# Performance work log

Measured on AMD Instinct MI355X. Metric: run time of the kernel, lower is better.

## Reference

```python
import jax, jax.numpy as jnp
import numpy as np

TOPK = 10
NUM_CLASSES = 80
ALPHA = 0.5
BETA = 6.0
EPS = 1e-9
IOU_EPS = 1e-7


def _make_anchors(img=640, strides=(8, 16, 32)):
    pts = []
    for s in strides:
        n = img // s
        ax = (np.arange(n, dtype=np.float32) + 0.5) * s
        gy, gx = np.meshgrid(ax, ax, indexing='ij')
        pts.append(np.stack([gx.ravel(), gy.ravel()], axis=-1))
    return jnp.asarray(np.concatenate(pts, axis=0), dtype=jnp.float32)  # [8400, 2]


def setup_inputs() -> dict:
    key = jax.random.key(0)
    ks = jax.random.split(key, 8)
    bs, ng, nc = 32, 64, NUM_CLASSES
    anc_points = _make_anchors()
    na = anc_points.shape[0]  # 8400
    pd_scores = jax.random.uniform(ks[0], (bs, na, nc), dtype=jnp.float32)
    pwh = jax.random.uniform(ks[1], (bs, na, 2), minval=10.0, maxval=100.0)
    pxy = anc_points[None] + jax.random.normal(ks[2], (bs, na, 2)) * 8.0
    pd_bboxes = jnp.concatenate([pxy - pwh / 2, pxy + pwh / 2], axis=-1)
    gxy = jax.random.uniform(ks[3], (bs, ng, 2), minval=50.0, maxval=590.0)
    gwh = jax.random.uniform(ks[4], (bs, ng, 2), minval=20.0, maxval=200.0)
    gt_bboxes = jnp.clip(jnp.concatenate([gxy - gwh / 2, gxy + gwh / 2], axis=-1), 0.0, 640.0)
    gt_labels = jax.random.randint(ks[5], (bs, ng, 1), 0, nc)
    num_gt = jax.random.randint(ks[6], (bs,), 1, ng + 1)
    mask_gt = (jnp.arange(ng)[None, :] < num_gt[:, None])[..., None]  # bool [bs, ng, 1]
    return {"pd_scores": pd_scores, "pd_bboxes": pd_bboxes, "anc_points": anc_points,
            "gt_labels": gt_labels, "gt_bboxes": gt_bboxes, "mask_gt": mask_gt}


def _iou_xyxy(b1, b2):
    # b1: [bs, na, 1, 4], b2: [bs, 1, ng, 4] -> [bs, na, ng]
    inter_w = jnp.maximum(jnp.minimum(b1[..., 2], b2[..., 2]) - jnp.maximum(b1[..., 0], b2[..., 0]), 0.0)
    inter_h = jnp.maximum(jnp.minimum(b1[..., 3], b2[..., 3]) - jnp.maximum(b1[..., 1], b2[..., 1]), 0.0)
    inter = inter_w * inter_h
    a1 = (b1[..., 2] - b1[..., 0]) * (b1[..., 3] - b1[..., 1])
    a2 = (b2[..., 2] - b2[..., 0]) * (b2[..., 3] - b2[..., 1])
    return inter / (a1 + a2 - inter + IOU_EPS)


def _assign(pd_scores, pd_bboxes, anc_points, gt_labels, gt_bboxes, mask_gt):
    bs, na, nc = pd_scores.shape
    ng = gt_bboxes.shape[1]
    dt = pd_scores.dtype

    # --- candidates whose center lies strictly inside the GT box ---
    lt = gt_bboxes[:, None, :, :2]          # [bs,1,ng,2]
    rb = gt_bboxes[:, None, :, 2:]
    xy = anc_points[None, :, None, :]       # [1,na,1,2]
    deltas = jnp.concatenate([xy - lt, rb - xy], axis=-1)  # [bs,na,ng,4]
    mask_in_gts = deltas.min(axis=-1) > EPS                 # [bs,na,ng]
    valid = mask_gt[..., 0].astype(bool)                    # [bs,ng]
    mask = mask_in_gts & valid[:, None, :]

    # --- alignment metric = score[label]^alpha * iou^beta, zeroed outside mask ---
    labels = gt_labels[..., 0].astype(jnp.int32)            # [bs,ng]
    idx = jnp.broadcast_to(labels[:, None, :], (bs, na, ng))
    gathered = jnp.take_along_axis(pd_scores, idx, axis=2)  # [bs,na,ng]
    bbox_scores = jnp.where(mask, gathered, 0.0)
    overlaps = jnp.where(mask, _iou_xyxy(pd_bboxes[:, :, None, :], gt_bboxes[:, None, :, :]), 0.0)
    safe_scores = jnp.where(mask, gathered, 1.0)  # avoids 0**0.5 grad issues; masked out below
    align_metric = jnp.where(mask, safe_scores ** ALPHA * overlaps ** BETA, 0.0)

    # --- top-k anchors per GT (over anchor dim) ---
    k = min(TOPK, na)
    _, topk_idx = jax.lax.top_k(jnp.swapaxes(align_metric, 1, 2), k)  # [bs,ng,k]
    bidx = jnp.arange(bs)[:, None, None]
    gidx = jnp.arange(ng)[None, :, None]
    in_topk = jnp.zeros((bs, ng, na), dtype=bool).at[bidx, gidx, topk_idx].set(True)
    in_topk = jnp.swapaxes(in_topk, 1, 2) & valid[:, None, :]  # [bs,na,ng]
    mask_pos = (in_topk & mask).astype(dt)

    # --- resolve anchors assigned to multiple GTs by highest IoU ---
    multi = mask_pos.sum(-1, keepdims=True) > 1
    is_max = jax.nn.one_hot(jnp.argmax(overlaps, axis=-1), ng, dtype=dt)
    mask_pos = jnp.where(multi, is_max, mask_pos)
    fg_mask = mask_pos.sum(-1) > 0                  # [bs,na] bool
    target_gt_idx = jnp.argmax(mask_pos, axis=-1)   # [bs,na]

    # --- gather targets ---
    flat_idx = target_gt_idx + jnp.arange(bs)[:, None] * ng
    target_labels = jnp.maximum(gt_labels[..., 0].reshape(-1)[flat_idx], 0)  # [bs,na]
    target_bboxes = gt_bboxes.reshape(-1, 4)[flat_idx]                       # [bs,na,4]
    one_hot = jax.nn.one_hot(target_labels, nc, dtype=dt) * fg_mask[..., None].astype(dt)

    fgf = fg_mask[..., None].astype(dt)
    norm_align = jnp.maximum((align_metric * fgf).max(-1, keepdims=True), EPS)
    norm_overlap = jnp.maximum((overlaps * fgf).max(-1, keepdims=True), EPS)
    t_scores = ((align_metric / norm_align) * (overlaps / norm_overlap) * fgf).max(-1)  # [bs,na]
    target_scores = one_hot * t_scores[..., None]
    return target_labels, target_bboxes, target_scores, fg_mask, target_gt_idx


def reference(pd_scores, pd_bboxes, anc_points, gt_labels, gt_bboxes, mask_gt):
    return _assign(pd_scores, pd_bboxes, anc_points, gt_labels, gt_bboxes, mask_gt)
```

## Files before the change

### kernel.cpp

```cpp
#include <hip/hip_runtime.h>
#include <math.h>

#define NC 80
#define TOPKK 10
#define EPSF 1e-9f
#define IOU_EPSF 1e-7f
#define NA 8400
#define NGMAX 64

__device__ __forceinline__ float iou_xyxy(float px0, float py0, float px1, float py1,
                                          float parea,
                                          float gx0, float gy0, float gx1, float gy1,
                                          float garea) {
    float iw = fmaxf(fminf(px1, gx1) - fmaxf(px0, gx0), 0.0f);
    float ih = fmaxf(fminf(py1, gy1) - fmaxf(py0, gy0), 0.0f);
    float inter = iw * ih;
    return inter / (parea + garea - inter + IOU_EPSF);
}

__device__ __forceinline__ float align_metric(float s, float ov) {
    float ov2 = ov * ov;
    return sqrtf(s) * (ov2 * ov2 * ov2);
}

__global__ __launch_bounds__(256) void topk_kernel(
    const float* __restrict__ pd_scores, const float* __restrict__ pd_bboxes,
    const float* __restrict__ anc, const int* __restrict__ gt_labels,
    const float* __restrict__ gt_bboxes, const int* __restrict__ mask_gt,
    unsigned long long* __restrict__ bits, int ng, int swz)
{
    __shared__ unsigned long long wkey[2][4];

    int b, g;
    if (swz) {
        int x = blockIdx.x & 7;
        int j = blockIdx.x >> 3;
        b = x * swz + j / ng;
        g = j - (j / ng) * ng;
    } else {
        b = blockIdx.x / ng;
        g = blockIdx.x - b * ng;
    }
    if (mask_gt[b * ng + g] == 0) return;

    int lab = gt_labels[b * ng + g];
    const float4 gb = ((const float4*)gt_bboxes)[b * ng + g];
    float gx0 = gb.x, gy0 = gb.y, gx1 = gb.z, gy1 = gb.w;
    float garea = (gx1 - gx0) * (gy1 - gy0);

    const float* __restrict__ srow = pd_scores + ((long)b * NA) * NC + lab;
    const float4* __restrict__ pbb = (const float4*)(pd_bboxes + (long)b * NA * 4);

    float lv[TOPKK];
    int   li[TOPKK];
#pragma unroll
    for (int j = 0; j < TOPKK; ++j) { lv[j] = -1.0f; li[j] = -1; }

    for (int a = threadIdx.x; a < NA; a += 256) {
        float ax = anc[a * 2 + 0];
        float ay = anc[a * 2 + 1];
        float d0 = ax - gx0, d1 = ay - gy0, d2 = gx1 - ax, d3 = gy1 - ay;
        float dmin = fminf(fminf(d0, d1), fminf(d2, d3));
        float v = 0.0f;
        if (dmin > EPSF) {
            float4 pb = pbb[a];
            float parea = (pb.z - pb.x) * (pb.w - pb.y);
            float ov = iou_xyxy(pb.x, pb.y, pb.z, pb.w, parea, gx0, gy0, gx1, gy1, garea);
            float s = srow[(long)a * NC];
            v = align_metric(s, ov);
        }
        if (v > lv[TOPKK - 1]) {
            float nv[TOPKK]; int ni[TOPKK];
#pragma unroll
            for (int j = 0; j < TOPKK; ++j) {
                bool keep = (lv[j] >= v);
                bool atp  = (j == 0) ? !keep : (!keep && (lv[j - 1] >= v));
                nv[j] = keep ? lv[j] : (atp ? v : lv[j - 1]);
                ni[j] = keep ? li[j] : (atp ? a : li[j - 1]);
            }
#pragma unroll
            for (int j = 0; j < TOPKK; ++j) { lv[j] = nv[j]; li[j] = ni[j]; }
        }
    }

    int lane = threadIdx.x & 63;
    int wid  = threadIdx.x >> 6;
    long bbase = (long)b * NA;

    for (int it = 0; it < TOPKK; ++it) {
        unsigned vb = __float_as_uint(lv[0]);
        unsigned long long myk = (lv[0] < 0.0f) ? 0ull
            : (((unsigned long long)vb << 32) | (unsigned)(~(unsigned)li[0]));

        unsigned long long k = myk;
#pragma unroll
        for (int off = 32; off > 0; off >>= 1) {
            unsigned long long o = __shfl_xor(k, off, 64);
            k = (o > k) ? o : k;
        }
        if (lane == 0) wkey[it & 1][wid] = k;
        __syncthreads();
        unsigned long long gk = wkey[it & 1][0];
        gk = (wkey[it & 1][1] > gk) ? wkey[it & 1][1] : gk;
        gk = (wkey[it & 1][2] > gk) ? wkey[it & 1][2] : gk;
        gk = (wkey[it & 1][3] > gk) ? wkey[it & 1][3] : gk;

        if (gk != 0ull && myk == gk) {
            atomicOr(&bits[bbase + li[0]], 1ull << g);
#pragma unroll
            for (int j = 0; j < TOPKK - 1; ++j) { lv[j] = lv[j + 1]; li[j] = li[j + 1]; }
            lv[TOPKK - 1] = -1.0f; li[TOPKK - 1] = -1;
        }
    }
}

__global__ __launch_bounds__(256) void assign_scores_kernel(
    const float* __restrict__ pd_scores, const float* __restrict__ pd_bboxes,
    const float* __restrict__ anc, const int* __restrict__ gt_labels,
    const float* __restrict__ gt_bboxes, const int* __restrict__ mask_gt,
    const unsigned long long* __restrict__ bits,
    float* __restrict__ out_labels, float* __restrict__ out_bboxes,
    float* __restrict__ out_scores, float* __restrict__ out_fg,
    float* __restrict__ out_tgt, int ng, int blocksPerB)
{
    __shared__ float4 sgt[NGMAX];
    __shared__ float  sarea[NGMAX];
    __shared__ int    slab[NGMAX];
    __shared__ int    svalid[NGMAX];
    __shared__ int    plab[256];
    __shared__ float  pt[256];

    int b  = blockIdx.x / blocksPerB;
    int a0 = (blockIdx.x - b * blocksPerB) * 256;
    int a  = a0 + threadIdx.x;

    for (int g = threadIdx.x; g < ng; g += 256) {
        float4 gb = ((const float4*)gt_bboxes)[b * ng + g];
        sgt[g] = gb;
        sarea[g] = (gb.z - gb.x) * (gb.w - gb.y);
        slab[g] = gt_labels[b * ng + g];
        svalid[g] = mask_gt[b * ng + g];
    }
    __syncthreads();

    bool alive = (a < NA);
    int labi = 0; float t = 0.0f;

    if (alive) {
        float ax = anc[a * 2 + 0];
        float ay = anc[a * 2 + 1];
        float4 pb = ((const float4*)pd_bboxes)[(long)b * NA + a];
        float parea = (pb.z - pb.x) * (pb.w - pb.y);
        unsigned long long w = bits[(long)b * NA + a];
        const float* __restrict__ srow = pd_scores + ((long)b * NA + a) * NC;

        int cnt = 0, pos_g = 0;
        float best_ov = 0.0f; int best_g = 0;
        float m_align = 0.0f, m_ov = 0.0f, t_raw = 0.0f;

        for (int g = 0; g < ng; ++g) {
            if (svalid[g] == 0) break;
            float4 gb = sgt[g];
            float d0 = ax - gb.x, d1 = ay - gb.y, d2 = gb.z - ax, d3 = gb.w - ay;
            float dmin = fminf(fminf(d0, d1), fminf(d2, d3));
            bool mask = (dmin > EPSF);
            float ov = 0.0f, al = 0.0f;
            if (mask) {
                ov = iou_xyxy(pb.x, pb.y, pb.z, pb.w, parea, gb.x, gb.y, gb.z, gb.w, sarea[g]);
                float s = srow[slab[g]];
                al = align_metric(s, ov);
            }
            bool pos = mask && ((w >> g) & 1ull);
            if (pos) { if (cnt == 0) pos_g = g; cnt++; }
            if (ov > best_ov) { best_ov = ov; best_g = g; }
            m_align = fmaxf(m_align, al);
            m_ov    = fmaxf(m_ov, ov);
            t_raw   = fmaxf(t_raw, al * ov);
        }

        int fg  = (cnt > 0) ? 1 : 0;
        int tgt = (cnt > 1) ? best_g : ((cnt == 1) ? pos_g : 0);

        labi = slab[tgt]; if (labi < 0) labi = 0;
        long ba = (long)b * NA + a;
        out_labels[ba] = (float)labi;
        ((float4*)out_bboxes)[ba] = sgt[tgt];
        out_fg[ba]  = (float)fg;
        out_tgt[ba] = (float)tgt;

        if (fg) {
            float na_ = fmaxf(m_align, EPSF);
            float no_ = fmaxf(m_ov, EPSF);
            t = (t_raw / na_) / no_;
        }
    }

    plab[threadIdx.x] = labi;
    pt[threadIdx.x]   = t;
    __syncthreads();

    int cnt_rows = NA - a0; if (cnt_rows > 256) cnt_rows = 256;
    int tot4 = cnt_rows * (NC / 4);
    float4* __restrict__ oslab = (float4*)(out_scores + ((long)b * NA + a0) * NC);
    for (int i = threadIdx.x; i < tot4; i += 256) {
        int al = i / (NC / 4);
        int cg = (i - al * (NC / 4)) * 4;
        int lab = plab[al];
        float tv = pt[al];
        float4 o;
        o.x = (cg     == lab) ? tv : 0.0f;
        o.y = (cg + 1 == lab) ? tv : 0.0f;
        o.z = (cg + 2 == lab) ? tv : 0.0f;
        o.w = (cg + 3 == lab) ? tv : 0.0f;
        oslab[i] = o;
    }
}

extern "C" void kernel_launch(void* const* d_in, const int* in_sizes, int n_in,
                              void* d_out, int out_size, void* d_ws, size_t ws_size,
                              hipStream_t stream) {
    const float* pd_scores = (const float*)d_in[0];
    const float* pd_bboxes = (const float*)d_in[1];
    const float* anc       = (const float*)d_in[2];
    const int*   gt_labels = (const int*)d_in[3];
    const float* gt_bboxes = (const float*)d_in[4];
    const int*   mask_gt   = (const int*)d_in[5];

    int na = in_sizes[2] / 2;
    int bs = in_sizes[0] / (na * NC);
    int ng = in_sizes[3] / bs;

    long nBA = (long)bs * na;
    float* out        = (float*)d_out;
    float* out_labels = out;
    float* out_bboxes = out + nBA;
    float* out_scores = out + nBA * 5;
    float* out_fg     = out + nBA * 85;
    float* out_tgt    = out + nBA * 86;

    unsigned long long* bits = (unsigned long long*)d_ws;

    hipMemsetAsync(d_ws, 0, nBA * sizeof(unsigned long long), stream);

    int swz = (bs % 8 == 0) ? (bs / 8) : 0;
    topk_kernel<<<bs * ng, 256, 0, stream>>>(
        pd_scores, pd_bboxes, anc, gt_labels, gt_bboxes, mask_gt, bits, ng, swz);

    int bpb = (na + 255) / 256;
    assign_scores_kernel<<<bs * bpb, 256, 0, stream>>>(
        pd_scores, pd_bboxes, anc, gt_labels, gt_bboxes, mask_gt, bits,
        out_labels, out_bboxes, out_scores, out_fg, out_tgt, ng, bpb);
}
```

Before: 205.3 us.

## Split top-k into anchor-chunk local selection plus per-GT merge phase

Replaces the per-(batch,GT) top-k kernel with two phases. The first phase stages a 128-anchor chunk of scores and boxes in shared memory and computes local top-10 lists for all 64 GTs at once. The second phase merges the per-chunk candidates with wave shuffles and sets the assignment bits. This removes 64 redundant strided passes over pd_scores per batch, at the cost of a large candidate buffer in workspace and an extra launch. The assign kernel also skips per-GT work for anchors with no bits set and uses nontemporal stores for the score tensor.

```diff
diff --git a/kernel.cpp b/kernel.cpp
--- a/kernel.cpp
+++ b/kernel.cpp
@@ -7,6 +7,10 @@
 #define IOU_EPSF 1e-7f
 #define NA 8400
 #define NGMAX 64
+#define CH 128
+#define NCH ((NA + CH - 1) / CH)
+
+typedef float f4nt __attribute__((ext_vector_type(4)));
 
 __device__ __forceinline__ float iou_xyxy(float px0, float py0, float px1, float py1,
                                           float parea,
@@ -22,6 +26,175 @@
     float ov2 = ov * ov;
     return sqrtf(s) * (ov2 * ov2 * ov2);
 }
+
+
+__global__ __launch_bounds__(256) void topk_phase1(
+    const float* __restrict__ pd_scores, const float* __restrict__ pd_bboxes,
+    const float* __restrict__ anc, const int* __restrict__ gt_labels,
+    const float* __restrict__ gt_bboxes, const int* __restrict__ mask_gt,
+    unsigned long long* __restrict__ cand, int ng)
+{
+    __shared__ union {
+        float sc[CH * NC];
+        unsigned long long mk[NGMAX * 4 * TOPKK];
+    } U;
+    __shared__ float4 sbb[CH];
+    __shared__ float2 sanc[CH];
+    __shared__ float4 sgt[NGMAX];
+    __shared__ int    slab[NGMAX];
+    __shared__ int    svalid[NGMAX];
+
+    int b  = blockIdx.x / NCH;
+    int c  = blockIdx.x - b * NCH;
+    int a0 = c * CH;
+    int rows = NA - a0; if (rows > CH) rows = CH;
+
+    for (int g = threadIdx.x; g < NGMAX; g += 256) {
+        if (g < ng) {
+            sgt[g]    = ((const float4*)gt_bboxes)[b * ng + g];
+            slab[g]   = gt_labels[b * ng + g];
+            svalid[g] = mask_gt[b * ng + g];
+        } else {
+            sgt[g] = make_float4(0, 0, 0, 0); slab[g] = 0; svalid[g] = 0;
+        }
+    }
+    for (int i = threadIdx.x; i < rows; i += 256) {
+        sbb[i]  = ((const float4*)pd_bboxes)[(long)b * NA + a0 + i];
+        sanc[i] = ((const float2*)anc)[a0 + i];
+    }
+    {
+        const float4* src = (const float4*)(pd_scores + ((long)b * NA + a0) * NC);
+        float4* dst = (float4*)U.sc;
+        int n4 = rows * (NC / 4);
+        for (int i = threadIdx.x; i < n4; i += 256) dst[i] = src[i];
+    }
+    __syncthreads();
+
+    int g   = threadIdx.x & 63;
+    int sub = threadIdx.x >> 6;
+
+    float lv[TOPKK]; int li[TOPKK];
+#pragma unroll
+    for (int j = 0; j < TOPKK; ++j) { lv[j] = -1.0f; li[j] = -1; }
+
+    if (svalid[g] != 0) {
+        float4 gb = sgt[g];
+        float garea = (gb.z - gb.x) * (gb.w - gb.y);
+        int lab = slab[g];
+        for (int al = sub; al < rows; al += 4) {
+            float2 ap = sanc[al];
+            float d0 = ap.x - gb.x, d1 = ap.y - gb.y, d2 = gb.z - ap.x, d3 = gb.w - ap.y;
+            float dmin = fminf(fminf(d0, d1), fminf(d2, d3));
+            float v = 0.0f;
+            if (dmin > EPSF) {
+                float4 pb = sbb[al];
+                float parea = (pb.z - pb.x) * (pb.w - pb.y);
+                float ov = iou_xyxy(pb.x, pb.y, pb.z, pb.w, parea,
+                                    gb.x, gb.y, gb.z, gb.w, garea);
+                float s = U.sc[al * NC + lab];
+                v = align_metric(s, ov);
+            }
+            if (v > lv[TOPKK - 1]) {
+                int a = a0 + al;
+                float nv[TOPKK]; int ni[TOPKK];
+#pragma unroll
+                for (int j = 0; j < TOPKK; ++j) {
+                    bool keep = (lv[j] >= v);
+                    bool atp  = (j == 0) ? !keep : (!keep && (lv[j - 1] >= v));
+                    nv[j] = keep ? lv[j] : (atp ? v : lv[j - 1]);
+                    ni[j] = keep ? li[j] : (atp ? a : li[j - 1]);
+                }
+#pragma unroll
+                for (int j = 0; j < TOPKK; ++j) { lv[j] = nv[j]; li[j] = ni[j]; }
+            }
+        }
+    }
+
+    __syncthreads();
+#pragma unroll
+    for (int j = 0; j < TOPKK; ++j) {
+        unsigned long long k = (lv[j] < 0.0f) ? 0ull
+            : (((unsigned long long)__float_as_uint(lv[j]) << 32)
+               | (unsigned)(~(unsigned)li[j]));
+        U.mk[(g * 4 + sub) * TOPKK + j] = k;
+    }
+    __syncthreads();
+
+    if (threadIdx.x < 64) {
+        int gg = threadIdx.x;
+        const unsigned long long* L = &U.mk[gg * 4 * TOPKK];
+        unsigned long long* outp = &cand[(((long)b * NCH + c) * 64 + gg) * TOPKK];
+        int p0 = 0, p1 = 0, p2 = 0, p3 = 0;
+#pragma unroll
+        for (int j = 0; j < TOPKK; ++j) {
+            unsigned long long k0 = L[0 * TOPKK + p0], k1 = L[1 * TOPKK + p1];
+            unsigned long long k2 = L[2 * TOPKK + p2], k3 = L[3 * TOPKK + p3];
+            unsigned long long bk = k0; int bi = 0;
+            if (k1 > bk) { bk = k1; bi = 1; }
+            if (k2 > bk) { bk = k2; bi = 2; }
+            if (k3 > bk) { bk = k3; bi = 3; }
+            outp[j] = bk;
+            if (bk != 0ull) {
+                if (bi == 0) p0++; else if (bi == 1) p1++;
+                else if (bi == 2) p2++; else p3++;
+            }
+        }
+    }
+}
+
+__global__ __launch_bounds__(64) void topk_phase2(
+    const unsigned long long* __restrict__ cand, const int* __restrict__ mask_gt,
+    unsigned long long* __restrict__ bits, int ng)
+{
+    int b = blockIdx.x / ng;
+    int g = blockIdx.x - b * ng;
+    if (mask_gt[b * ng + g] == 0) return;
+    int lane = threadIdx.x;
+
+    unsigned long long A[TOPKK], B[TOPKK], M[TOPKK];
+    {
+        const unsigned long long* p = &cand[(((long)b * NCH + lane) * 64 + g) * TOPKK];
+#pragma unroll
+        for (int j = 0; j < TOPKK; ++j) A[j] = p[j];
+    }
+    int c2 = lane + 64;
+    if (c2 < NCH) {
+        const unsigned long long* p = &cand[(((long)b * NCH + c2) * 64 + g) * TOPKK];
+#pragma unroll
+        for (int j = 0; j < TOPKK; ++j) B[j] = p[j];
+    } else {
+#pragma unroll
+        for (int j = 0; j < TOPKK; ++j) B[j] = 0ull;
+    }
+    {
+        int pa = 0, pb = 0;
+#pragma unroll
+        for (int j = 0; j < TOPKK; ++j) {
+            unsigned long long ka = A[pa], kb = B[pb];
+            if (ka >= kb) { M[j] = ka; if (ka != 0ull) pa++; }
+            else          { M[j] = kb; pb++; }
+        }
+    }
+
+    int pos = 0;
+    long bbase = (long)b * NA;
+    for (int it = 0; it < TOPKK; ++it) {
+        unsigned long long myk = (pos < TOPKK) ? M[pos] : 0ull;
+        unsigned long long k = myk;
+#pragma unroll
+        for (int off = 32; off > 0; off >>= 1) {
+            unsigned long long o = __shfl_xor(k, off, 64);
+            k = (o > k) ? o : k;
+        }
+        if (k == 0ull) break;
+        if (myk == k) {
+            unsigned idx = ~(unsigned)k;
+            atomicOr(&bits[bbase + idx], 1ull << g);
+            pos++;
+        }
+    }
+}
+
 
 __global__ __launch_bounds__(256) void topk_kernel(
     const float* __restrict__ pd_scores, const float* __restrict__ pd_bboxes,
@@ -51,8 +224,7 @@
     const float* __restrict__ srow = pd_scores + ((long)b * NA) * NC + lab;
     const float4* __restrict__ pbb = (const float4*)(pd_bboxes + (long)b * NA * 4);
 
-    float lv[TOPKK];
-    int   li[TOPKK];
+    float lv[TOPKK]; int li[TOPKK];
 #pragma unroll
     for (int j = 0; j < TOPKK; ++j) { lv[j] = -1.0f; li[j] = -1; }
 
@@ -113,6 +285,7 @@
         }
     }
 }
+
 
 __global__ __launch_bounds__(256) void assign_scores_kernel(
     const float* __restrict__ pd_scores, const float* __restrict__ pd_bboxes,
@@ -144,54 +317,63 @@
     __syncthreads();
 
     bool alive = (a < NA);
-    int labi = 0; float t = 0.0f;
+    int labi0 = slab[0] < 0 ? 0 : slab[0];
+    int labi = labi0; float t = 0.0f;
 
     if (alive) {
-        float ax = anc[a * 2 + 0];
-        float ay = anc[a * 2 + 1];
-        float4 pb = ((const float4*)pd_bboxes)[(long)b * NA + a];
-        float parea = (pb.z - pb.x) * (pb.w - pb.y);
-        unsigned long long w = bits[(long)b * NA + a];
-        const float* __restrict__ srow = pd_scores + ((long)b * NA + a) * NC;
-
-        int cnt = 0, pos_g = 0;
-        float best_ov = 0.0f; int best_g = 0;
-        float m_align = 0.0f, m_ov = 0.0f, t_raw = 0.0f;
-
-        for (int g = 0; g < ng; ++g) {
-            if (svalid[g] == 0) break;
-            float4 gb = sgt[g];
-            float d0 = ax - gb.x, d1 = ay - gb.y, d2 = gb.z - ax, d3 = gb.w - ay;
-            float dmin = fminf(fminf(d0, d1), fminf(d2, d3));
-            bool mask = (dmin > EPSF);
-            float ov = 0.0f, al = 0.0f;
-            if (mask) {
-                ov = iou_xyxy(pb.x, pb.y, pb.z, pb.w, parea, gb.x, gb.y, gb.z, gb.w, sarea[g]);
-                float s = srow[slab[g]];
-                al = align_metric(s, ov);
-            }
-            bool pos = mask && ((w >> g) & 1ull);
-            if (pos) { if (cnt == 0) pos_g = g; cnt++; }
-            if (ov > best_ov) { best_ov = ov; best_g = g; }
-            m_align = fmaxf(m_align, al);
-            m_ov    = fmaxf(m_ov, ov);
-            t_raw   = fmaxf(t_raw, al * ov);
-        }
-
-        int fg  = (cnt > 0) ? 1 : 0;
-        int tgt = (cnt > 1) ? best_g : ((cnt == 1) ? pos_g : 0);
-
-        labi = slab[tgt]; if (labi < 0) labi = 0;
         long ba = (long)b * NA + a;
-        out_labels[ba] = (float)labi;
-        ((float4*)out_bboxes)[ba] = sgt[tgt];
-        out_fg[ba]  = (float)fg;
-        out_tgt[ba] = (float)tgt;
-
-        if (fg) {
-            float na_ = fmaxf(m_align, EPSF);
-            float no_ = fmaxf(m_ov, EPSF);
-            t = (t_raw / na_) / no_;
+        unsigned long long w = bits[ba];
+        if (w == 0ull) {
+            out_labels[ba] = (float)labi0;
+            ((float4*)out_bboxes)[ba] = sgt[0];
+            out_fg[ba]  = 0.0f;
+            out_tgt[ba] = 0.0f;
+        } else {
+            float ax = anc[a * 2 + 0];
+            float ay = anc[a * 2 + 1];
+            float4 pb = ((const float4*)pd_bboxes)[ba];
+            float parea = (pb.z - pb.x) * (pb.w - pb.y);
+            const float* __restrict__ srow = pd_scores + ba * NC;
+
+            int cnt = 0, pos_g = 0;
+            float best_ov = 0.0f; int best_g = 0;
+            float m_align = 0.0f, m_ov = 0.0f, t_raw = 0.0f;
+
+            for (int g = 0; g < ng; ++g) {
+                if (svalid[g] == 0) break;
+                float4 gb = sgt[g];
+                float d0 = ax - gb.x, d1 = ay - gb.y, d2 = gb.z - ax, d3 = gb.w - ay;
+                float dmin = fminf(fminf(d0, d1), fminf(d2, d3));
+                bool mask = (dmin > EPSF);
+                float ov = 0.0f, al = 0.0f;
+                if (mask) {
+                    ov = iou_xyxy(pb.x, pb.y, pb.z, pb.w, parea,
+                                  gb.x, gb.y, gb.z, gb.w, sarea[g]);
+                    float s = srow[slab[g]];
+                    al = align_metric(s, ov);
+                }
+                bool pos = mask && ((w >> g) & 1ull);
+                if (pos) { if (cnt == 0) pos_g = g; cnt++; }
+                if (ov > best_ov) { best_ov = ov; best_g = g; }
+                m_align = fmaxf(m_align, al);
+                m_ov    = fmaxf(m_ov, ov);
+                t_raw   = fmaxf(t_raw, al * ov);
+            }
+
+            int fg  = (cnt > 0) ? 1 : 0;
+            int tgt = (cnt > 1) ? best_g : ((cnt == 1) ? pos_g : 0);
+
+            labi = slab[tgt]; if (labi < 0) labi = 0;
+            out_labels[ba] = (float)labi;
+            ((float4*)out_bboxes)[ba] = sgt[tgt];
+            out_fg[ba]  = (float)fg;
+            out_tgt[ba] = (float)tgt;
+
+            if (fg) {
+                float na_ = fmaxf(m_align, EPSF);
+                float no_ = fmaxf(m_ov, EPSF);
+                t = (t_raw / na_) / no_;
+            }
         }
     }
 
@@ -201,18 +383,18 @@
 
     int cnt_rows = NA - a0; if (cnt_rows > 256) cnt_rows = 256;
     int tot4 = cnt_rows * (NC / 4);
-    float4* __restrict__ oslab = (float4*)(out_scores + ((long)b * NA + a0) * NC);
+    f4nt* __restrict__ oslab = (f4nt*)(out_scores + ((long)b * NA + a0) * NC);
     for (int i = threadIdx.x; i < tot4; i += 256) {
         int al = i / (NC / 4);
         int cg = (i - al * (NC / 4)) * 4;
         int lab = plab[al];
         float tv = pt[al];
-        float4 o;
+        f4nt o;
         o.x = (cg     == lab) ? tv : 0.0f;
         o.y = (cg + 1 == lab) ? tv : 0.0f;
         o.z = (cg + 2 == lab) ? tv : 0.0f;
         o.w = (cg + 3 == lab) ? tv : 0.0f;
-        oslab[i] = o;
+        __builtin_nontemporal_store(o, &oslab[i]);
     }
 }
 
@@ -239,12 +421,21 @@
     float* out_tgt    = out + nBA * 86;
 
     unsigned long long* bits = (unsigned long long*)d_ws;
+    unsigned long long* cand = bits + nBA;
+
+    size_t need = (size_t)nBA * 8 + (size_t)bs * NCH * 64 * TOPKK * 8;
 
     hipMemsetAsync(d_ws, 0, nBA * sizeof(unsigned long long), stream);
 
-    int swz = (bs % 8 == 0) ? (bs / 8) : 0;
-    topk_kernel<<<bs * ng, 256, 0, stream>>>(
-        pd_scores, pd_bboxes, anc, gt_labels, gt_bboxes, mask_gt, bits, ng, swz);
+    if (ws_size >= need) {
+        topk_phase1<<<bs * NCH, 256, 0, stream>>>(
+            pd_scores, pd_bboxes, anc, gt_labels, gt_bboxes, mask_gt, cand, ng);
+        topk_phase2<<<bs * ng, 64, 0, stream>>>(cand, mask_gt, bits, ng);
+    } else {
+        int swz = (bs % 8 == 0) ? (bs / 8) : 0;
+        topk_kernel<<<bs * ng, 256, 0, stream>>>(
+            pd_scores, pd_bboxes, anc, gt_labels, gt_bboxes, mask_gt, bits, ng, swz);
+    }
 
     int bpb = (na + 255) / 256;
     assign_scores_kernel<<<bs * bpb, 256, 0, stream>>>(
```

Measured after the change: 243.6 us. +18.6%, slower.

## Restrict top-k scan to anchor rectangle inside each GT box, one wave per GT

Applied to the files above, without the earlier changes.

The top-k kernel now computes, for each of the three stride levels, the rectangle of anchor grid cells that can fall inside the GT box, and scans only those anchors with a single 64-lane wave per (batch, GT) pair instead of a 256-thread block over all 8400 anchors. This drops the cross-wave LDS reduction and the barriers. A serial fallback reproduces the reference tie behaviour when fewer than k positive candidates exist, by picking the lowest-index zero-metric anchors. The assign kernel also skips the per-GT loop for anchors with no candidate bits, and the dense score output uses nontemporal stores. The risks are the anchor-geometry assumptions baked in as constants and the slow serial fallback for small boxes.

```diff
diff --git a/kernel.cpp b/kernel.cpp
--- a/kernel.cpp
+++ b/kernel.cpp
@@ -7,6 +7,8 @@
 #define IOU_EPSF 1e-7f
 #define NA 8400
 #define NGMAX 64
+
+typedef float f4nt __attribute__((ext_vector_type(4)));
 
 __device__ __forceinline__ float iou_xyxy(float px0, float py0, float px1, float py1,
                                           float parea,
@@ -23,93 +25,127 @@
     return sqrtf(s) * (ov2 * ov2 * ov2);
 }
 
-__global__ __launch_bounds__(256) void topk_kernel(
+__global__ __launch_bounds__(256) void topk_rect_kernel(
     const float* __restrict__ pd_scores, const float* __restrict__ pd_bboxes,
-    const float* __restrict__ anc, const int* __restrict__ gt_labels,
-    const float* __restrict__ gt_bboxes, const int* __restrict__ mask_gt,
-    unsigned long long* __restrict__ bits, int ng, int swz)
+    const int* __restrict__ gt_labels, const float* __restrict__ gt_bboxes,
+    const int* __restrict__ mask_gt,
+    unsigned long long* __restrict__ bits, int ng, int total_bg)
 {
-    __shared__ unsigned long long wkey[2][4];
-
-    int b, g;
-    if (swz) {
-        int x = blockIdx.x & 7;
-        int j = blockIdx.x >> 3;
-        b = x * swz + j / ng;
-        g = j - (j / ng) * ng;
-    } else {
-        b = blockIdx.x / ng;
-        g = blockIdx.x - b * ng;
-    }
+    int lin = blockIdx.x * 4 + (threadIdx.x >> 6);
+    if (lin >= total_bg) return;
+    int b = lin / ng;
+    int g = lin - b * ng;
     if (mask_gt[b * ng + g] == 0) return;
+    int lane = threadIdx.x & 63;
 
     int lab = gt_labels[b * ng + g];
-    const float4 gb = ((const float4*)gt_bboxes)[b * ng + g];
-    float gx0 = gb.x, gy0 = gb.y, gx1 = gb.z, gy1 = gb.w;
-    float garea = (gx1 - gx0) * (gy1 - gy0);
-
+    float4 gb = ((const float4*)gt_bboxes)[b * ng + g];
+    float garea = (gb.z - gb.x) * (gb.w - gb.y);
     const float* __restrict__ srow = pd_scores + ((long)b * NA) * NC + lab;
     const float4* __restrict__ pbb = (const float4*)(pd_bboxes + (long)b * NA * 4);
 
-    float lv[TOPKK];
-    int   li[TOPKK];
+    const int ls[3] = {8, 16, 32};
+    const int ln[3] = {80, 40, 20};
+    const int lb[3] = {0, 6400, 8000};
+    int jlo[3], ilo[3], rw[3], cnt[3];
+    int tot = 0;
+#pragma unroll
+    for (int l = 0; l < 3; ++l) {
+        float s = (float)ls[l];
+        int j0 = (int)floorf(gb.x / s - 0.5f) - 1; if (j0 < 0) j0 = 0;
+        int j1 = (int)ceilf (gb.z / s - 0.5f) + 1; if (j1 > ln[l] - 1) j1 = ln[l] - 1;
+        int i0 = (int)floorf(gb.y / s - 0.5f) - 1; if (i0 < 0) i0 = 0;
+        int i1 = (int)ceilf (gb.w / s - 0.5f) + 1; if (i1 > ln[l] - 1) i1 = ln[l] - 1;
+        int w = j1 - j0 + 1; if (w < 0) w = 0;
+        int h = i1 - i0 + 1; if (h < 0) h = 0;
+        jlo[l] = j0; ilo[l] = i0; rw[l] = w; cnt[l] = w * h; tot += cnt[l];
+    }
+
+    float lv[TOPKK]; int li[TOPKK];
 #pragma unroll
     for (int j = 0; j < TOPKK; ++j) { lv[j] = -1.0f; li[j] = -1; }
 
-    for (int a = threadIdx.x; a < NA; a += 256) {
-        float ax = anc[a * 2 + 0];
-        float ay = anc[a * 2 + 1];
-        float d0 = ax - gx0, d1 = ay - gy0, d2 = gx1 - ax, d3 = gy1 - ay;
+    for (int t = lane; t < tot; t += 64) {
+        int l = 0, r = t;
+        if (r >= cnt[0]) { r -= cnt[0]; l = 1; }
+        if (l == 1 && r >= cnt[1]) { r -= cnt[1]; l = 2; }
+        int i  = r / rw[l];
+        int j  = r - i * rw[l];
+        int ii = ilo[l] + i, jj = jlo[l] + j;
+        int a  = lb[l] + ii * ln[l] + jj;
+        float s  = (float)ls[l];
+        float ax = (jj + 0.5f) * s, ay = (ii + 0.5f) * s;
+        float d0 = ax - gb.x, d1 = ay - gb.y, d2 = gb.z - ax, d3 = gb.w - ay;
         float dmin = fminf(fminf(d0, d1), fminf(d2, d3));
-        float v = 0.0f;
         if (dmin > EPSF) {
             float4 pb = pbb[a];
             float parea = (pb.z - pb.x) * (pb.w - pb.y);
-            float ov = iou_xyxy(pb.x, pb.y, pb.z, pb.w, parea, gx0, gy0, gx1, gy1, garea);
-            float s = srow[(long)a * NC];
-            v = align_metric(s, ov);
-        }
-        if (v > lv[TOPKK - 1]) {
-            float nv[TOPKK]; int ni[TOPKK];
-#pragma unroll
-            for (int j = 0; j < TOPKK; ++j) {
-                bool keep = (lv[j] >= v);
-                bool atp  = (j == 0) ? !keep : (!keep && (lv[j - 1] >= v));
-                nv[j] = keep ? lv[j] : (atp ? v : lv[j - 1]);
-                ni[j] = keep ? li[j] : (atp ? a : li[j - 1]);
-            }
-#pragma unroll
-            for (int j = 0; j < TOPKK; ++j) { lv[j] = nv[j]; li[j] = ni[j]; }
-        }
-    }
-
-    int lane = threadIdx.x & 63;
-    int wid  = threadIdx.x >> 6;
+            float ov = iou_xyxy(pb.x, pb.y, pb.z, pb.w, parea,
+                                gb.x, gb.y, gb.z, gb.w, garea);
+            float sc = srow[(long)a * NC];
+            float v = align_metric(sc, ov);
+            if (v > 0.0f && v > lv[TOPKK - 1]) {
+                float nv[TOPKK]; int ni[TOPKK];
+#pragma unroll
+                for (int q = 0; q < TOPKK; ++q) {
+                    bool keep = (lv[q] >= v);
+                    bool atp  = (q == 0) ? !keep : (!keep && (lv[q - 1] >= v));
+                    nv[q] = keep ? lv[q] : (atp ? v : lv[q - 1]);
+                    ni[q] = keep ? li[q] : (atp ? a : li[q - 1]);
+                }
+#pragma unroll
+                for (int q = 0; q < TOPKK; ++q) { lv[q] = nv[q]; li[q] = ni[q]; }
+            }
+        }
+    }
+
     long bbase = (long)b * NA;
-
+    int m = 0;
     for (int it = 0; it < TOPKK; ++it) {
-        unsigned vb = __float_as_uint(lv[0]);
-        unsigned long long myk = (lv[0] < 0.0f) ? 0ull
-            : (((unsigned long long)vb << 32) | (unsigned)(~(unsigned)li[0]));
-
+        unsigned long long myk = (lv[0] > 0.0f)
+            ? (((unsigned long long)__float_as_uint(lv[0]) << 32)
+               | (unsigned)(~(unsigned)li[0]))
+            : 0ull;
         unsigned long long k = myk;
 #pragma unroll
         for (int off = 32; off > 0; off >>= 1) {
             unsigned long long o = __shfl_xor(k, off, 64);
             k = (o > k) ? o : k;
         }
-        if (lane == 0) wkey[it & 1][wid] = k;
-        __syncthreads();
-        unsigned long long gk = wkey[it & 1][0];
-        gk = (wkey[it & 1][1] > gk) ? wkey[it & 1][1] : gk;
-        gk = (wkey[it & 1][2] > gk) ? wkey[it & 1][2] : gk;
-        gk = (wkey[it & 1][3] > gk) ? wkey[it & 1][3] : gk;
-
-        if (gk != 0ull && myk == gk) {
+        if (k == 0ull) break;
+        if (myk == k) {
             atomicOr(&bits[bbase + li[0]], 1ull << g);
 #pragma unroll
-            for (int j = 0; j < TOPKK - 1; ++j) { lv[j] = lv[j + 1]; li[j] = li[j + 1]; }
+            for (int q = 0; q < TOPKK - 1; ++q) { lv[q] = lv[q + 1]; li[q] = li[q + 1]; }
             lv[TOPKK - 1] = -1.0f; li[TOPKK - 1] = -1;
+        }
+        m++;
+    }
+
+    if (m < TOPKK && lane == 0) {
+        int need = TOPKK - m;
+        for (int a = 0; need > 0 && a < NA; ++a) {
+            int l  = (a < 6400) ? 0 : ((a < 8000) ? 1 : 2);
+            int rr = a - lb[l];
+            int ii = rr / ln[l];
+            int jj = rr - ii * ln[l];
+            float s  = (float)ls[l];
+            float ax = (jj + 0.5f) * s, ay = (ii + 0.5f) * s;
+            float d0 = ax - gb.x, d1 = ay - gb.y, d2 = gb.z - ax, d3 = gb.w - ay;
+            float dmin = fminf(fminf(d0, d1), fminf(d2, d3));
+            bool positive = false;
+            if (dmin > EPSF) {
+                float4 pb = pbb[a];
+                float parea = (pb.z - pb.x) * (pb.w - pb.y);
+                float ov = iou_xyxy(pb.x, pb.y, pb.z, pb.w, parea,
+                                    gb.x, gb.y, gb.z, gb.w, garea);
+                float sc = srow[(long)a * NC];
+                positive = (align_metric(sc, ov) > 0.0f);
+            }
+            if (!positive) {
+                atomicOr(&bits[bbase + a], 1ull << g);
+                need--;
+            }
         }
     }
 }
@@ -144,54 +180,63 @@
     __syncthreads();
 
     bool alive = (a < NA);
-    int labi = 0; float t = 0.0f;
+    int labi0 = slab[0] < 0 ? 0 : slab[0];
+    int labi = labi0; float t = 0.0f;
 
     if (alive) {
-        float ax = anc[a * 2 + 0];
-        float ay = anc[a * 2 + 1];
-        float4 pb = ((const float4*)pd_bboxes)[(long)b * NA + a];
-        float parea = (pb.z - pb.x) * (pb.w - pb.y);
-        unsigned long long w = bits[(long)b * NA + a];
-        const float* __restrict__ srow = pd_scores + ((long)b * NA + a) * NC;
-
-        int cnt = 0, pos_g = 0;
-        float best_ov = 0.0f; int best_g = 0;
-        float m_align = 0.0f, m_ov = 0.0f, t_raw = 0.0f;
-
-        for (int g = 0; g < ng; ++g) {
-            if (svalid[g] == 0) break;
-            float4 gb = sgt[g];
-            float d0 = ax - gb.x, d1 = ay - gb.y, d2 = gb.z - ax, d3 = gb.w - ay;
-            float dmin = fminf(fminf(d0, d1), fminf(d2, d3));
-            bool mask = (dmin > EPSF);
-            float ov = 0.0f, al = 0.0f;
-            if (mask) {
-                ov = iou_xyxy(pb.x, pb.y, pb.z, pb.w, parea, gb.x, gb.y, gb.z, gb.w, sarea[g]);
-                float s = srow[slab[g]];
-                al = align_metric(s, ov);
-            }
-            bool pos = mask && ((w >> g) & 1ull);
-            if (pos) { if (cnt == 0) pos_g = g; cnt++; }
-            if (ov > best_ov) { best_ov = ov; best_g = g; }
-            m_align = fmaxf(m_align, al);
-            m_ov    = fmaxf(m_ov, ov);
-            t_raw   = fmaxf(t_raw, al * ov);
-        }
-
-        int fg  = (cnt > 0) ? 1 : 0;
-        int tgt = (cnt > 1) ? best_g : ((cnt == 1) ? pos_g : 0);
-
-        labi = slab[tgt]; if (labi < 0) labi = 0;
         long ba = (long)b * NA + a;
-        out_labels[ba] = (float)labi;
-        ((float4*)out_bboxes)[ba] = sgt[tgt];
-        out_fg[ba]  = (float)fg;
-        out_tgt[ba] = (float)tgt;
-
-        if (fg) {
-            float na_ = fmaxf(m_align, EPSF);
-            float no_ = fmaxf(m_ov, EPSF);
-            t = (t_raw / na_) / no_;
+        unsigned long long w = bits[ba];
+        if (w == 0ull) {
+            out_labels[ba] = (float)labi0;
+            ((float4*)out_bboxes)[ba] = sgt[0];
+            out_fg[ba]  = 0.0f;
+            out_tgt[ba] = 0.0f;
+        } else {
+            float ax = anc[a * 2 + 0];
+            float ay = anc[a * 2 + 1];
+            float4 pb = ((const float4*)pd_bboxes)[ba];
+            float parea = (pb.z - pb.x) * (pb.w - pb.y);
+            const float* __restrict__ srow = pd_scores + ba * NC;
+
+            int cnt = 0, pos_g = 0;
+            float best_ov = 0.0f; int best_g = 0;
+            float m_align = 0.0f, m_ov = 0.0f, t_raw = 0.0f;
+
+            for (int g = 0; g < ng; ++g) {
+                if (svalid[g] == 0) break;
+                float4 gb = sgt[g];
+                float d0 = ax - gb.x, d1 = ay - gb.y, d2 = gb.z - ax, d3 = gb.w - ay;
+                float dmin = fminf(fminf(d0, d1), fminf(d2, d3));
+                bool mask = (dmin > EPSF);
+                float ov = 0.0f, al = 0.0f;
+                if (mask) {
+                    ov = iou_xyxy(pb.x, pb.y, pb.z, pb.w, parea,
+                                  gb.x, gb.y, gb.z, gb.w, sarea[g]);
+                    float s = srow[slab[g]];
+                    al = align_metric(s, ov);
+                }
+                bool pos = mask && ((w >> g) & 1ull);
+                if (pos) { if (cnt == 0) pos_g = g; cnt++; }
+                if (ov > best_ov) { best_ov = ov; best_g = g; }
+                m_align = fmaxf(m_align, al);
+                m_ov    = fmaxf(m_ov, ov);
+                t_raw   = fmaxf(t_raw, al * ov);
+            }
+
+            int fg  = (cnt > 0) ? 1 : 0;
+            int tgt = (cnt > 1) ? best_g : ((cnt == 1) ? pos_g : 0);
+
+            labi = slab[tgt]; if (labi < 0) labi = 0;
+            out_labels[ba] = (float)labi;
+            ((float4*)out_bboxes)[ba] = sgt[tgt];
+            out_fg[ba]  = (float)fg;
+            out_tgt[ba] = (float)tgt;
+
+            if (fg) {
+                float na_ = fmaxf(m_align, EPSF);
+                float no_ = fmaxf(m_ov, EPSF);
+                t = (t_raw / na_) / no_;
+            }
         }
     }
 
@@ -201,18 +246,18 @@
 
     int cnt_rows = NA - a0; if (cnt_rows > 256) cnt_rows = 256;
     int tot4 = cnt_rows * (NC / 4);
-    float4* __restrict__ oslab = (float4*)(out_scores + ((long)b * NA + a0) * NC);
+    f4nt* __restrict__ oslab = (f4nt*)(out_scores + ((long)b * NA + a0) * NC);
     for (int i = threadIdx.x; i < tot4; i += 256) {
         int al = i / (NC / 4);
         int cg = (i - al * (NC / 4)) * 4;
         int lab = plab[al];
         float tv = pt[al];
-        float4 o;
+        f4nt o;
         o.x = (cg     == lab) ? tv : 0.0f;
         o.y = (cg + 1 == lab) ? tv : 0.0f;
         o.z = (cg + 2 == lab) ? tv : 0.0f;
         o.w = (cg + 3 == lab) ? tv : 0.0f;
-        oslab[i] = o;
+        __builtin_nontemporal_store(o, &oslab[i]);
     }
 }
 
@@ -242,9 +287,10 @@
 
     hipMemsetAsync(d_ws, 0, nBA * sizeof(unsigned long long), stream);
 
-    int swz = (bs % 8 == 0) ? (bs / 8) : 0;
-    topk_kernel<<<bs * ng, 256, 0, stream>>>(
-        pd_scores, pd_bboxes, anc, gt_labels, gt_bboxes, mask_gt, bits, ng, swz);
+    int total_bg = bs * ng;
+    int nblk = (total_bg + 3) / 4;
+    topk_rect_kernel<<<nblk, 256, 0, stream>>>(
+        pd_scores, pd_bboxes, gt_labels, gt_bboxes, mask_gt, bits, ng, total_bg);
 
     int bpb = (na + 255) / 256;
     assign_scores_kernel<<<bs * bpb, 256, 0, stream>>>(
```

Result: faster. 200.3 us (-2.4%).
